# Performance work log

Hardware: AMD Instinct MI355X
Metric: run time of the kernel (lower is better)

Reference implementation:

```python
import jax, jax.numpy as jnp
import numpy as np

D_MODEL = 1024
EXPAND = 2
D_INNER = D_MODEL * EXPAND  # 2048 independent SSM channels
D_STATE = 16
BATCH = 4
SEQ = 4096


def setup_inputs() -> dict:
    key = jax.random.key(0)
    ks = jax.random.split(key, 10)
    w = lambda k, shape, scale=0.02: jax.random.normal(k, shape, jnp.float32) * scale
    return {
        "x": jax.random.normal(ks[0], (BATCH, SEQ, D_MODEL), jnp.float32),
        "w_in": w(ks[1], (D_MODEL, D_INNER)),
        "b_in": jnp.zeros((D_INNER,), jnp.float32),
        "w_gate": w(ks[2], (D_MODEL, D_INNER)),
        "b_gate": jnp.zeros((D_INNER,), jnp.float32),
        # per-channel linear SSM params: h_t = A h_{t-1} + B x_t ; y_t = C . h_t
        "A": w(ks[3], (D_INNER, D_STATE, D_STATE), 0.05),  # small spectral radius -> stable recurrence
        "B_ssm": w(ks[4], (D_INNER, D_STATE), 0.1),
        "C_ssm": w(ks[5], (D_INNER, D_STATE), 0.1),
        "w_out": w(ks[6], (D_INNER, D_MODEL)),
        "b_out": jnp.zeros((D_MODEL,), jnp.float32),
    }


def reference(x, w_in, b_in, w_gate, b_gate, A, B_ssm, C_ssm, w_out, b_out):
    # x: [B, S, D]
    x_proj = x @ w_in + b_in                     # [B, S, C]
    gate = jax.nn.sigmoid(x @ w_gate + b_gate)   # [B, S, C]

    def step(h, xt):
        # h: [B, C, N] state for all channels; xt: [B, C] scalar input per channel
        h = jnp.einsum("cnm,bcm->bcn", A, h) + B_ssm[None] * xt[:, :, None]
        y = jnp.einsum("bcn,cn->bc", h, C_ssm)
        return h, y

    h0 = jnp.zeros((x.shape[0], D_INNER, D_STATE), x.dtype)
    xs = jnp.swapaxes(x_proj, 0, 1)              # [S, B, C]
    _, ys = jax.lax.scan(step, h0, xs)           # ys: [S, B, C]
    ssm_out = jnp.swapaxes(ys, 0, 1)             # [B, S, C]

    y = ssm_out * gate
    return y @ w_out + b_out                     # [B, S, D]
```

## Files before the change

### kernel.cpp

```cpp
#include <hip/hip_runtime.h>
#include <hip/hip_bf16.h>

#define D_MODEL 1024
#define D_INNER 2048
#define D_STATE 16
#define BATCH   4
#define SEQ     4096
#define MROWS   (BATCH * SEQ)

#define LTAPS 16
#define TSPAN 64

using bf16 = __hip_bfloat16;

typedef __attribute__((ext_vector_type(8))) short bf16x8;
typedef __attribute__((ext_vector_type(4))) float f32x4;

__device__ __forceinline__ float bf2f(bf16 v) { return __bfloat162float(v); }
__device__ __forceinline__ unsigned short f2bfbits(float f) {
  bf16 h = __float2bfloat16(f);
  return *(unsigned short*)&h;
}
__device__ __forceinline__ float bfbits2f(unsigned short u) {
  union { float f; unsigned int i; } x; x.i = (unsigned int)u << 16; return x.f;
}

#define AS1CAST(p) ((const __attribute__((address_space(1))) unsigned int*)(unsigned long long)(p))
#define AS3CAST(p) ((__attribute__((address_space(3))) unsigned int*)(unsigned long long)(p))

#define FENCE() asm volatile("" ::: "memory")
#define BAR() do { FENCE(); __builtin_amdgcn_s_barrier(); FENCE(); } while (0)
#define PRIO1 __builtin_amdgcn_s_setprio(1)
#define PRIO0 __builtin_amdgcn_s_setprio(0)

#define TILE_E (256 * 64)

struct G8 {
  const bf16 *gA, *gB;
  size_t K64, K128;
  int stageLds;
  int baseA0, baseA1;
  int baseB0, baseB1;
  int wr, wc, lane;
};

__device__ __forceinline__ void g8_setup(G8& g, const bf16* A, const bf16* BT,
                                         int m0, int n0, int K)
{
  const int tid = threadIdx.x;
  g.lane = tid & 63;
  const int wv = tid >> 6;
  g.wr = wv >> 2;
  g.wc = wv & 3;
  const int lr = g.lane >> 3, sl = g.lane & 7;
  g.gA = A  + (size_t)(m0 + wv * 8 + lr) * K + (sl ^ lr) * 8;
  g.gB = BT + (size_t)(n0 + wv * 8 + lr) * K + (sl ^ lr) * 8;
  g.K64  = (size_t)64 * K;
  g.K128 = (size_t)128 * K;
  g.stageLds = wv * 8 * 64;
  const int fla = g.lane & 15, cb = g.lane >> 4;
  const int s0 = cb ^ (fla & 7), s1 = s0 ^ 4;
  g.baseA0 = (g.wr * 64 + fla) * 64 + s0 * 8;
  g.baseA1 = (g.wr * 64 + fla) * 64 + s1 * 8;
  g.baseB0 = (g.wc * 32 + fla) * 64 + s0 * 8;
  g.baseB1 = (g.wc * 32 + fla) * 64 + s1 * 8;
}

__device__ __forceinline__ void g8_stageA(const G8& g, bf16* dstTile, int h, int tau)
{
  const bf16* s = g.gA + (h ? g.K128 : (size_t)0) + (size_t)tau * 64;
  bf16* d = dstTile + g.stageLds + h * (128 * 64);
  __builtin_amdgcn_global_load_lds(AS1CAST(s), AS3CAST(d), 16, 0, 0);
  __builtin_amdgcn_global_load_lds(AS1CAST(s + g.K64), AS3CAST(d + 64 * 64), 16, 0, 0);
}

__device__ __forceinline__ void g8_stageB(const G8& g, bf16* dstTile, int h, int tau)
{
  const bf16* s = g.gB + (h ? g.K128 : (size_t)0) + (size_t)tau * 64;
  bf16* d = dstTile + g.stageLds + h * (128 * 64);
  __builtin_amdgcn_global_load_lds(AS1CAST(s), AS3CAST(d), 16, 0, 0);
  __builtin_amdgcn_global_load_lds(AS1CAST(s + g.K64), AS3CAST(d + 64 * 64), 16, 0, 0);
}

__device__ __forceinline__ void rdA(bf16x8 (&d)[4], const bf16* T, int base, int mh)
{
#pragma unroll
  for (int mi = 0; mi < 4; ++mi)
    d[mi] = *(const bf16x8*)&T[base + mh * 8192 + mi * 1024];
}
__device__ __forceinline__ void rdB(bf16x8 (&d)[2], const bf16* T, int base, int nh)
{
#pragma unroll
  for (int ni = 0; ni < 2; ++ni)
    d[ni] = *(const bf16x8*)&T[base + nh * 8192 + ni * 1024];
}

#define MQS(MH, NH, AF, BF) do { _Pragma("unroll") \
  for (int mi = 0; mi < 4; ++mi) { _Pragma("unroll") \
    for (int ni = 0; ni < 2; ++ni) \
      acc[MH][NH][mi][ni] = __builtin_amdgcn_mfma_f32_16x16x32_bf16( \
          (AF)[mi], (BF)[ni], acc[MH][NH][mi][ni], 0, 0, 0); \
  } } while (0)

template<bool MORE>
__device__ __forceinline__ void g8_tile(const G8& g, const bf16* At, const bf16* Bt,
    bf16* An, bf16* Bn, int t, f32x4 (&acc)[2][2][4][2],
    bf16x8 (&aP)[4], bf16x8 (&aQ)[4], bf16x8 (&b0s0)[2], bf16x8 (&b0s1)[2],
    bf16x8 (&b1s0)[2], bf16x8 (&b1s1)[2])
{
  rdA(aQ, At, g.baseA1, 0);
  if constexpr (MORE) g8_stageA(g, An, 0, t + 1);
  PRIO1; MQS(0, 0, aP, b0s0); PRIO0;
  rdB(b1s0, Bt, g.baseB0, 1);
  if constexpr (MORE) g8_stageB(g, Bn, 0, t + 1);
  PRIO1; MQS(0, 0, aQ, b0s1); PRIO0;
  rdB(b1s1, Bt, g.baseB1, 1);
  if constexpr (MORE) g8_stageA(g, An, 1, t + 1);
  PRIO1; MQS(0, 1, aP, b1s0); PRIO0;
  rdA(aP, At, g.baseA0, 1);
  if constexpr (MORE) g8_stageB(g, Bn, 1, t + 1);
  PRIO1; MQS(0, 1, aQ, b1s1); PRIO0;
  rdA(aQ, At, g.baseA1, 1);
  PRIO1; MQS(1, 1, aP, b1s0); PRIO0;
  PRIO1; MQS(1, 1, aQ, b1s1); PRIO0;
  PRIO1; MQS(1, 0, aP, b0s0); PRIO0;
  if constexpr (MORE) {
    asm volatile("s_waitcnt vmcnt(0)" ::: "memory");
    BAR();
  }
  PRIO1; MQS(1, 0, aQ, b0s1); PRIO0;
  if constexpr (MORE) {
    rdA(aP, An, g.baseA0, 0);
    rdB(b0s0, Bn, g.baseB0, 0);
    rdB(b0s1, Bn, g.baseB1, 0);
  }
}

__device__ __forceinline__ void g8_main(const G8& g, bf16* As, bf16* Bs,
                                        f32x4 (&acc)[2][2][4][2], int K)
{
  const int nt = K >> 6;
  bf16* A0 = As; bf16* A1 = As + TILE_E;
  bf16* B0 = Bs; bf16* B1 = Bs + TILE_E;

  g8_stageA(g, A0, 0, 0);
  g8_stageB(g, B0, 0, 0);
  g8_stageA(g, A0, 1, 0);
  g8_stageB(g, B0, 1, 0);
  asm volatile("s_waitcnt vmcnt(0)" ::: "memory");
  BAR();

  bf16x8 aP[4], aQ[4], b0s0[2], b0s1[2], b1s0[2], b1s1[2];
  rdA(aP, A0, g.baseA0, 0);
  rdB(b0s0, B0, g.baseB0, 0);
  rdB(b0s1, B0, g.baseB1, 0);

  for (int t = 0; t < nt - 1; ++t) {
    bf16* At = (t & 1) ? A1 : A0;
    bf16* Bt = (t & 1) ? B1 : B0;
    bf16* An = (t & 1) ? A0 : A1;
    bf16* Bn = (t & 1) ? B0 : B1;
    g8_tile<true>(g, At, Bt, An, Bn, t, acc, aP, aQ, b0s0, b0s1, b1s0, b1s1);
  }
  bf16* At = ((nt - 1) & 1) ? A1 : A0;
  bf16* Bt = ((nt - 1) & 1) ? B1 : B0;
  g8_tile<false>(g, At, Bt, At, Bt, nt - 1, acc, aP, aQ, b0s0, b0s1, b1s0, b1s1);
}

__global__ __launch_bounds__(512, 2) void gemm_proj_dual(
    const bf16* __restrict__ A,
    const bf16* __restrict__ BT,
    const float* __restrict__ bias_in, const float* __restrict__ bias_gate,
    bf16* __restrict__ xp, bf16* __restrict__ gate)
{
  __shared__ alignas(16) bf16 As[2 * TILE_E];
  __shared__ alignas(16) bf16 Bs[2 * TILE_E];

  const int b = blockIdx.x;
  const int swz = (b & 7) * 128 + (b >> 3);
  const int bm = swz >> 4, bn = swz & 15;
  const int m0 = bm * 256, n0 = bn * 256;

  G8 g;
  g8_setup(g, A, BT, m0, n0, D_MODEL);

  f32x4 acc[2][2][4][2];
#pragma unroll
  for (int a1 = 0; a1 < 2; ++a1)
#pragma unroll
    for (int a2 = 0; a2 < 2; ++a2)
#pragma unroll
      for (int a3 = 0; a3 < 4; ++a3)
#pragma unroll
        for (int a4 = 0; a4 < 2; ++a4)
          acc[a1][a2][a3][a4] = (f32x4){0.f, 0.f, 0.f, 0.f};

  g8_main(g, As, Bs, acc, D_MODEL);

  const bool isGate = (n0 >= D_INNER);
  const int  nloc0  = n0 - (isGate ? D_INNER : 0);
  const float* bias = isGate ? bias_gate : bias_in;
  bf16* dst         = isGate ? gate : xp;

  const int crow = (g.lane >> 4) * 4;
  const int ccol = g.lane & 15;
#pragma unroll
  for (int mh = 0; mh < 2; ++mh)
#pragma unroll
    for (int nh = 0; nh < 2; ++nh)
#pragma unroll
      for (int mi = 0; mi < 4; ++mi)
#pragma unroll
        for (int ni = 0; ni < 2; ++ni) {
          const int col = nloc0 + nh * 128 + g.wc * 32 + ni * 16 + ccol;
          const float bcol = bias[col];
#pragma unroll
          for (int r = 0; r < 4; ++r) {
            const size_t row = (size_t)(m0 + mh * 128 + g.wr * 64 + mi * 16 + crow + r);
            float v = acc[mh][nh][mi][ni][r] + bcol;
            if (isGate) v = 1.0f / (1.0f + __expf(-v));
            dst[row * D_INNER + col] = __float2bfloat16(v);
          }
        }
}

__global__ __launch_bounds__(512, 2) void gemm_out(
    const bf16* __restrict__ A,
    const bf16* __restrict__ BT,
    const float* __restrict__ bias,
    float* __restrict__ C)
{
  __shared__ alignas(16) bf16 As[2 * TILE_E];
  __shared__ alignas(16) bf16 Bs[2 * TILE_E];

  const int b = blockIdx.x;
  const int swz = (b & 7) * 32 + (b >> 3);
  const int bm = swz >> 2, bn = swz & 3;
  const int m0 = bm * 256, n0 = bn * 256;

  G8 g;
  g8_setup(g, A, BT, m0, n0, D_INNER);

  f32x4 acc[2][2][4][2];
#pragma unroll
  for (int a1 = 0; a1 < 2; ++a1)
#pragma unroll
    for (int a2 = 0; a2 < 2; ++a2)
#pragma unroll
      for (int a3 = 0; a3 < 4; ++a3)
#pragma unroll
        for (int a4 = 0; a4 < 2; ++a4)
          acc[a1][a2][a3][a4] = (f32x4){0.f, 0.f, 0.f, 0.f};

  g8_main(g, As, Bs, acc, D_INNER);

  const int crow = (g.lane >> 4) * 4;
  const int ccol = g.lane & 15;
#pragma unroll
  for (int mh = 0; mh < 2; ++mh)
#pragma unroll
    for (int nh = 0; nh < 2; ++nh)
#pragma unroll
      for (int mi = 0; mi < 4; ++mi)
#pragma unroll
        for (int ni = 0; ni < 2; ++ni) {
          const int col = n0 + nh * 128 + g.wc * 32 + ni * 16 + ccol;
          const float bcol = bias[col];
#pragma unroll
          for (int r = 0; r < 4; ++r) {
            const size_t row = (size_t)(m0 + mh * 128 + g.wr * 64 + mi * 16 + crow + r);
            C[row * D_MODEL + col] = acc[mh][nh][mi][ni][r] + bcol;
          }
        }
}

__global__ __launch_bounds__(256) void f32_to_bf16(
    const float* __restrict__ in, bf16* __restrict__ out, int n4)
{
  const int i = (blockIdx.x * 256 + threadIdx.x);
  if (i >= n4) return;
  const float4 v = *(const float4*)(in + (size_t)i * 4);
  ushort4 r;
  r.x = f2bfbits(v.x); r.y = f2bfbits(v.y); r.z = f2bfbits(v.z); r.w = f2bfbits(v.w);
  *(ushort4*)(out + (size_t)i * 4) = r;
}

__global__ __launch_bounds__(256) void transpose_to_bf16(
    const float* __restrict__ in, bf16* __restrict__ out, int R, int C)
{
  __shared__ float tile[32][33];
  const int c0 = blockIdx.x * 32, r0 = blockIdx.y * 32;
  const int tx = threadIdx.x & 31, ty = threadIdx.x >> 5;
#pragma unroll
  for (int i = ty; i < 32; i += 8)
    tile[i][tx] = in[(size_t)(r0 + i) * C + c0 + tx];
  __syncthreads();
#pragma unroll
  for (int i = ty; i < 32; i += 8)
    out[(size_t)(c0 + i) * R + r0 + tx] = __float2bfloat16(tile[tx][i]);
}

__device__ __forceinline__ float4 load4f(const float* p) { return *(const float4*)p; }

__global__ __launch_bounds__(256) void ssm_taps(
    const float* __restrict__ A, const float* __restrict__ Bv,
    const float* __restrict__ Cv, float* __restrict__ g)
{
  const int c = blockIdx.x * blockDim.x + threadIdx.x;
  if (c >= D_INNER) return;
  const float* Ac = A + (size_t)c * D_STATE * D_STATE;
  float v[D_STATE], cr[D_STATE];
#pragma unroll
  for (int i = 0; i < D_STATE; ++i) {
    v[i]  = Bv[(size_t)c * D_STATE + i];
    cr[i] = Cv[(size_t)c * D_STATE + i];
  }
  for (int m = 0; m < LTAPS; ++m) {
    float y = 0.f;
#pragma unroll
    for (int i = 0; i < D_STATE; ++i) y += cr[i] * v[i];
    g[(size_t)m * D_INNER + c] = y;
    float nv[D_STATE];
#pragma unroll
    for (int n = 0; n < D_STATE; ++n) {
      const float4 a0 = load4f(Ac + n * D_STATE + 0);
      const float4 a1 = load4f(Ac + n * D_STATE + 4);
      const float4 a2 = load4f(Ac + n * D_STATE + 8);
      const float4 a3 = load4f(Ac + n * D_STATE + 12);
      float s = a0.x * v[0] + a0.y * v[1] + a0.z * v[2] + a0.w * v[3];
      s += a1.x * v[4] + a1.y * v[5] + a1.z * v[6] + a1.w * v[7];
      s += a2.x * v[8] + a2.y * v[9] + a2.z * v[10] + a2.w * v[11];
      s += a3.x * v[12] + a3.y * v[13] + a3.z * v[14] + a3.w * v[15];
      nv[n] = s;
    }
#pragma unroll
    for (int i = 0; i < D_STATE; ++i) v[i] = nv[i];
  }
}

__global__ __launch_bounds__(256) void conv_gate(
    const bf16* __restrict__ xp, bf16* __restrict__ gate_io,
    const float* __restrict__ g)
{
  const int cp = blockIdx.x * blockDim.x + threadIdx.x;
  const int c  = cp * 2;
  const int b  = blockIdx.z;
  const int t0 = blockIdx.y * TSPAN;

  float gg0[LTAPS], gg1[LTAPS];
#pragma unroll
  for (int m = 0; m < LTAPS; ++m) {
    gg0[m] = g[(size_t)m * D_INNER + c];
    gg1[m] = g[(size_t)m * D_INNER + c + 1];
  }

  const size_t baseBC = ((size_t)b * SEQ) * D_INNER + c;

  float w0[2 * LTAPS], w1[2 * LTAPS];
#pragma unroll
  for (int j = 0; j < LTAPS; ++j) {
    const int t = t0 - LTAPS + j;
    if (t >= 0) {
      const ushort2 v = *(const ushort2*)&xp[baseBC + (size_t)t * D_INNER];
      w0[j] = bfbits2f(v.x); w1[j] = bfbits2f(v.y);
    } else { w0[j] = 0.f; w1[j] = 0.f; }
  }

  for (int blk = 0; blk < TSPAN; blk += LTAPS) {
#pragma unroll
    for (int j = 0; j < LTAPS; ++j) {
      const ushort2 v = *(const ushort2*)&xp[baseBC + (size_t)(t0 + blk + j) * D_INNER];
      w0[LTAPS + j] = bfbits2f(v.x); w1[LTAPS + j] = bfbits2f(v.y);
    }
#pragma unroll
    for (int j = 0; j < LTAPS; ++j) {
      float y0 = 0.f, y1 = 0.f;
#pragma unroll
      for (int m = 0; m < LTAPS; ++m) {
        y0 += gg0[m] * w0[LTAPS + j - m];
        y1 += gg1[m] * w1[LTAPS + j - m];
      }
      const size_t idx = baseBC + (size_t)(t0 + blk + j) * D_INNER;
      const unsigned int gv = *(const unsigned int*)&gate_io[idx];
      const float g0 = bfbits2f((unsigned short)(gv & 0xffffu));
      const float g1 = bfbits2f((unsigned short)(gv >> 16));
      const unsigned int ov =
          (unsigned int)f2bfbits(y0 * g0) | ((unsigned int)f2bfbits(y1 * g1) << 16);
      *(unsigned int*)&gate_io[idx] = ov;
    }
#pragma unroll
    for (int j = 0; j < LTAPS; ++j) { w0[j] = w0[j + LTAPS]; w1[j] = w1[j + LTAPS]; }
  }
}

extern "C" void kernel_launch(void* const* d_in, const int* in_sizes, int n_in,
                              void* d_out, int out_size, void* d_ws, size_t ws_size,
                              hipStream_t stream)
{
  const float* x      = (const float*)d_in[0];
  const float* w_in   = (const float*)d_in[1];
  const float* b_in   = (const float*)d_in[2];
  const float* w_gate = (const float*)d_in[3];
  const float* b_gate = (const float*)d_in[4];
  const float* A      = (const float*)d_in[5];
  const float* B_ssm  = (const float*)d_in[6];
  const float* C_ssm  = (const float*)d_in[7];
  const float* w_out  = (const float*)d_in[8];
  const float* b_out  = (const float*)d_in[9];
  float* out = (float*)d_out;

  char* ws = (char*)d_ws;
  bf16*  gate  = (bf16*)(ws);
  bf16*  xbf   = (bf16*)(ws + 67108864);
  bf16*  wcatT = (bf16*)(ws + 100663296);
  bf16*  w_otT = (bf16*)(ws + 109051904);
  float* taps  = (float*)(ws + 113246208);
  bf16*  xp    = (bf16*)d_out;

  dim3 blk(256);

  hipLaunchKernelGGL(ssm_taps, dim3(D_INNER / 256), blk, 0, stream, A, B_ssm, C_ssm, taps);
  hipLaunchKernelGGL(f32_to_bf16, dim3((MROWS * D_MODEL / 4) / 256), blk, 0, stream,
                     x, xbf, MROWS * D_MODEL / 4);
  hipLaunchKernelGGL(transpose_to_bf16, dim3(D_INNER / 32, D_MODEL / 32), blk, 0, stream,
                     w_in, wcatT, D_MODEL, D_INNER);
  hipLaunchKernelGGL(transpose_to_bf16, dim3(D_INNER / 32, D_MODEL / 32), blk, 0, stream,
                     w_gate, wcatT + (size_t)D_INNER * D_MODEL, D_MODEL, D_INNER);
  hipLaunchKernelGGL(transpose_to_bf16, dim3(D_MODEL / 32, D_INNER / 32), blk, 0, stream,
                     w_out, w_otT, D_INNER, D_MODEL);

  dim3 gblk(512);
  hipLaunchKernelGGL(gemm_proj_dual, dim3((2 * D_INNER / 256) * (MROWS / 256)), gblk, 0, stream,
                     xbf, wcatT, b_in, b_gate, xp, gate);

  dim3 gc(D_INNER / 2 / 256, SEQ / TSPAN, BATCH);
  hipLaunchKernelGGL(conv_gate, gc, blk, 0, stream, xp, gate, taps);

  hipLaunchKernelGGL(gemm_out, dim3((D_MODEL / 256) * (MROWS / 256)), gblk, 0, stream,
                     gate, w_otT, b_out, out);
}
```

Before: 391.0 us.

## Load GEMM B fragments directly from global into registers with 4-stage A ring

Both GEMM kernels stop staging the B operand through LDS and instead load each wave's B fragments straight from global memory into registers one K-step ahead. The A tile gets a 4-deep LDS ring with a prefetch distance of two, and a barrier only every second K-step. Launch bounds drop to one block per CU. The aim is to halve LDS traffic and cut barriers, at the cost of uncoalesced, redundant global reads of B across waves, higher register pressure and lower occupancy.

```diff
diff --git a/kernel.cpp b/kernel.cpp
--- a/kernel.cpp
+++ b/kernel.cpp
@@ -33,14 +33,14 @@
 #define PRIO1 __builtin_amdgcn_s_setprio(1)
 #define PRIO0 __builtin_amdgcn_s_setprio(0)
 
-#define TILE_E (256 * 64)
+#define TILE_A 16384
 
 struct G8 {
-  const bf16 *gA, *gB;
-  size_t K64, K128;
+  const bf16 *gA;
+  const bf16 *gBF;
+  size_t K64;
   int stageLds;
   int baseA0, baseA1;
-  int baseB0, baseB1;
   int wr, wc, lane;
 };
 
@@ -53,33 +53,35 @@
   g.wr = wv >> 2;
   g.wc = wv & 3;
   const int lr = g.lane >> 3, sl = g.lane & 7;
-  g.gA = A  + (size_t)(m0 + wv * 8 + lr) * K + (sl ^ lr) * 8;
-  g.gB = BT + (size_t)(n0 + wv * 8 + lr) * K + (sl ^ lr) * 8;
-  g.K64  = (size_t)64 * K;
-  g.K128 = (size_t)128 * K;
+  g.gA = A + (size_t)(m0 + wv * 8 + lr) * K + (sl ^ lr) * 8;
+  g.K64 = (size_t)64 * K;
   g.stageLds = wv * 8 * 64;
   const int fla = g.lane & 15, cb = g.lane >> 4;
-  const int s0 = cb ^ (fla & 7), s1 = s0 ^ 4;
+  const int s0 = cb ^ (fla & 7);
   g.baseA0 = (g.wr * 64 + fla) * 64 + s0 * 8;
-  g.baseA1 = (g.wr * 64 + fla) * 64 + s1 * 8;
-  g.baseB0 = (g.wc * 32 + fla) * 64 + s0 * 8;
-  g.baseB1 = (g.wc * 32 + fla) * 64 + s1 * 8;
-}
-
-__device__ __forceinline__ void g8_stageA(const G8& g, bf16* dstTile, int h, int tau)
-{
-  const bf16* s = g.gA + (h ? g.K128 : (size_t)0) + (size_t)tau * 64;
-  bf16* d = dstTile + g.stageLds + h * (128 * 64);
-  __builtin_amdgcn_global_load_lds(AS1CAST(s), AS3CAST(d), 16, 0, 0);
-  __builtin_amdgcn_global_load_lds(AS1CAST(s + g.K64), AS3CAST(d + 64 * 64), 16, 0, 0);
-}
-
-__device__ __forceinline__ void g8_stageB(const G8& g, bf16* dstTile, int h, int tau)
-{
-  const bf16* s = g.gB + (h ? g.K128 : (size_t)0) + (size_t)tau * 64;
-  bf16* d = dstTile + g.stageLds + h * (128 * 64);
-  __builtin_amdgcn_global_load_lds(AS1CAST(s), AS3CAST(d), 16, 0, 0);
-  __builtin_amdgcn_global_load_lds(AS1CAST(s + g.K64), AS3CAST(d + 64 * 64), 16, 0, 0);
+  g.baseA1 = (g.wr * 64 + fla) * 64 + (s0 ^ 4) * 8;
+  g.gBF = BT + (size_t)(n0 + g.wc * 32 + fla) * K + cb * 8;
+}
+
+__device__ __forceinline__ void g8_stageA(const G8& g, bf16* dstTile, int tau)
+{
+  const bf16* s = g.gA + (size_t)tau * 64;
+  bf16* d = dstTile + g.stageLds;
+  __builtin_amdgcn_global_load_lds(AS1CAST(s),             AS3CAST(d),         16, 0, 0);
+  __builtin_amdgcn_global_load_lds(AS1CAST(s + g.K64),     AS3CAST(d + 4096),  16, 0, 0);
+  __builtin_amdgcn_global_load_lds(AS1CAST(s + 2 * g.K64), AS3CAST(d + 8192),  16, 0, 0);
+  __builtin_amdgcn_global_load_lds(AS1CAST(s + 3 * g.K64), AS3CAST(d + 12288), 16, 0, 0);
+}
+
+template<int S>
+__device__ __forceinline__ void loadBs(const G8& g, bf16x8 (&B)[2][2][2], int t, int K)
+{
+#pragma unroll
+  for (int nh = 0; nh < 2; ++nh)
+#pragma unroll
+    for (int ni = 0; ni < 2; ++ni)
+      B[S][nh][ni] = *(const bf16x8*)(g.gBF + (size_t)(nh * 128 + ni * 16) * K
+                                      + (size_t)t * 64 + S * 32);
 }
 
 __device__ __forceinline__ void rdA(bf16x8 (&d)[4], const bf16* T, int base, int mh)
@@ -88,93 +90,71 @@
   for (int mi = 0; mi < 4; ++mi)
     d[mi] = *(const bf16x8*)&T[base + mh * 8192 + mi * 1024];
 }
-__device__ __forceinline__ void rdB(bf16x8 (&d)[2], const bf16* T, int base, int nh)
-{
-#pragma unroll
-  for (int ni = 0; ni < 2; ++ni)
-    d[ni] = *(const bf16x8*)&T[base + nh * 8192 + ni * 1024];
-}
-
-#define MQS(MH, NH, AF, BF) do { _Pragma("unroll") \
-  for (int mi = 0; mi < 4; ++mi) { _Pragma("unroll") \
-    for (int ni = 0; ni < 2; ++ni) \
-      acc[MH][NH][mi][ni] = __builtin_amdgcn_mfma_f32_16x16x32_bf16( \
-          (AF)[mi], (BF)[ni], acc[MH][NH][mi][ni], 0, 0, 0); \
-  } } while (0)
-
-template<bool MORE>
-__device__ __forceinline__ void g8_tile(const G8& g, const bf16* At, const bf16* Bt,
-    bf16* An, bf16* Bn, int t, f32x4 (&acc)[2][2][4][2],
-    bf16x8 (&aP)[4], bf16x8 (&aQ)[4], bf16x8 (&b0s0)[2], bf16x8 (&b0s1)[2],
-    bf16x8 (&b1s0)[2], bf16x8 (&b1s1)[2])
-{
-  rdA(aQ, At, g.baseA1, 0);
-  if constexpr (MORE) g8_stageA(g, An, 0, t + 1);
-  PRIO1; MQS(0, 0, aP, b0s0); PRIO0;
-  rdB(b1s0, Bt, g.baseB0, 1);
-  if constexpr (MORE) g8_stageB(g, Bn, 0, t + 1);
-  PRIO1; MQS(0, 0, aQ, b0s1); PRIO0;
-  rdB(b1s1, Bt, g.baseB1, 1);
-  if constexpr (MORE) g8_stageA(g, An, 1, t + 1);
-  PRIO1; MQS(0, 1, aP, b1s0); PRIO0;
-  rdA(aP, At, g.baseA0, 1);
-  if constexpr (MORE) g8_stageB(g, Bn, 1, t + 1);
-  PRIO1; MQS(0, 1, aQ, b1s1); PRIO0;
-  rdA(aQ, At, g.baseA1, 1);
-  PRIO1; MQS(1, 1, aP, b1s0); PRIO0;
-  PRIO1; MQS(1, 1, aQ, b1s1); PRIO0;
-  PRIO1; MQS(1, 0, aP, b0s0); PRIO0;
-  if constexpr (MORE) {
-    asm volatile("s_waitcnt vmcnt(0)" ::: "memory");
-    BAR();
-  }
-  PRIO1; MQS(1, 0, aQ, b0s1); PRIO0;
-  if constexpr (MORE) {
-    rdA(aP, An, g.baseA0, 0);
-    rdB(b0s0, Bn, g.baseB0, 0);
-    rdB(b0s1, Bn, g.baseB1, 0);
-  }
-}
-
-__device__ __forceinline__ void g8_main(const G8& g, bf16* As, bf16* Bs,
+
+#define MQ2(MH, S, AF, BB) do { _Pragma("unroll") \
+  for (int nh = 0; nh < 2; ++nh) { _Pragma("unroll") \
+    for (int mi = 0; mi < 4; ++mi) { _Pragma("unroll") \
+      for (int ni = 0; ni < 2; ++ni) \
+        acc[MH][nh][mi][ni] = __builtin_amdgcn_mfma_f32_16x16x32_bf16( \
+            (AF)[mi], (BB)[S][nh][ni], acc[MH][nh][mi][ni], 0, 0, 0); \
+  } } } while (0)
+
+template<bool LB, bool ST, bool BARR, bool NXT, int BCUR, int BSTG, int BNXT>
+__device__ __forceinline__ void g8_t(const G8& g, bf16* As, int t, int K,
+    f32x4 (&acc)[2][2][4][2], bf16x8 (&aP)[4], bf16x8 (&aQ)[4],
+    bf16x8 (&Bb)[2][2][2])
+{
+  const bf16* Tc = As + BCUR;
+  rdA(aQ, Tc, g.baseA1, 0);
+  if constexpr (ST) g8_stageA(g, As + BSTG, t + 2);
+  PRIO1; MQ2(0, 0, aP, Bb); PRIO0;
+  rdA(aP, Tc, g.baseA0, 1);
+  PRIO1; MQ2(0, 1, aQ, Bb); PRIO0;
+  rdA(aQ, Tc, g.baseA1, 1);
+  PRIO1; MQ2(1, 0, aP, Bb); PRIO0;
+  if constexpr (LB) loadBs<0>(g, Bb, t + 1, K);
+  if constexpr (BARR) { asm volatile("s_waitcnt vmcnt(0)" ::: "memory"); BAR(); }
+  PRIO1; MQ2(1, 1, aQ, Bb); PRIO0;
+  if constexpr (LB) loadBs<1>(g, Bb, t + 1, K);
+  if constexpr (NXT) rdA(aP, As + BNXT, g.baseA0, 0);
+}
+
+__device__ __forceinline__ void g8_main(const G8& g, bf16* As,
                                         f32x4 (&acc)[2][2][4][2], int K)
 {
   const int nt = K >> 6;
-  bf16* A0 = As; bf16* A1 = As + TILE_E;
-  bf16* B0 = Bs; bf16* B1 = Bs + TILE_E;
-
-  g8_stageA(g, A0, 0, 0);
-  g8_stageB(g, B0, 0, 0);
-  g8_stageA(g, A0, 1, 0);
-  g8_stageB(g, B0, 1, 0);
+  bf16x8 Bb[2][2][2];
+
+  g8_stageA(g, As,          0);
+  g8_stageA(g, As + TILE_A, 1);
+  loadBs<0>(g, Bb, 0, K);
+  loadBs<1>(g, Bb, 0, K);
   asm volatile("s_waitcnt vmcnt(0)" ::: "memory");
   BAR();
 
-  bf16x8 aP[4], aQ[4], b0s0[2], b0s1[2], b1s0[2], b1s1[2];
-  rdA(aP, A0, g.baseA0, 0);
-  rdB(b0s0, B0, g.baseB0, 0);
-  rdB(b0s1, B0, g.baseB1, 0);
-
-  for (int t = 0; t < nt - 1; ++t) {
-    bf16* At = (t & 1) ? A1 : A0;
-    bf16* Bt = (t & 1) ? B1 : B0;
-    bf16* An = (t & 1) ? A0 : A1;
-    bf16* Bn = (t & 1) ? B0 : B1;
-    g8_tile<true>(g, At, Bt, An, Bn, t, acc, aP, aQ, b0s0, b0s1, b1s0, b1s1);
-  }
-  bf16* At = ((nt - 1) & 1) ? A1 : A0;
-  bf16* Bt = ((nt - 1) & 1) ? B1 : B0;
-  g8_tile<false>(g, At, Bt, At, Bt, nt - 1, acc, aP, aQ, b0s0, b0s1, b1s0, b1s1);
-}
-
-__global__ __launch_bounds__(512, 2) void gemm_proj_dual(
+  bf16x8 aP[4], aQ[4];
+  rdA(aP, As, g.baseA0, 0);
+
+  int t = 0;
+  for (; t < nt - 4; t += 4) {
+    g8_t<true, true, false, true, 0,     32768, 16384>(g, As, t + 0, K, acc, aP, aQ, Bb);
+    g8_t<true, true, true,  true, 16384, 49152, 32768>(g, As, t + 1, K, acc, aP, aQ, Bb);
+    g8_t<true, true, false, true, 32768, 0,     49152>(g, As, t + 2, K, acc, aP, aQ, Bb);
+    g8_t<true, true, true,  true, 49152, 16384, 0    >(g, As, t + 3, K, acc, aP, aQ, Bb);
+  }
+  g8_t<true,  true,  false, true,  0,     32768, 16384>(g, As, t + 0, K, acc, aP, aQ, Bb);
+  g8_t<true,  true,  true,  true,  16384, 49152, 32768>(g, As, t + 1, K, acc, aP, aQ, Bb);
+  g8_t<true,  false, false, true,  32768, 0,     49152>(g, As, t + 2, K, acc, aP, aQ, Bb);
+  g8_t<false, false, false, false, 49152, 0,     0    >(g, As, t + 3, K, acc, aP, aQ, Bb);
+}
+
+__global__ __launch_bounds__(512, 1) void gemm_proj_dual(
     const bf16* __restrict__ A,
     const bf16* __restrict__ BT,
     const float* __restrict__ bias_in, const float* __restrict__ bias_gate,
     bf16* __restrict__ xp, bf16* __restrict__ gate)
 {
-  __shared__ alignas(16) bf16 As[2 * TILE_E];
-  __shared__ alignas(16) bf16 Bs[2 * TILE_E];
+  __shared__ alignas(16) bf16 As[4 * TILE_A];
 
   const int b = blockIdx.x;
   const int swz = (b & 7) * 128 + (b >> 3);
@@ -195,7 +175,7 @@
         for (int a4 = 0; a4 < 2; ++a4)
           acc[a1][a2][a3][a4] = (f32x4){0.f, 0.f, 0.f, 0.f};
 
-  g8_main(g, As, Bs, acc, D_MODEL);
+  g8_main(g, As, acc, D_MODEL);
 
   const bool isGate = (n0 >= D_INNER);
   const int  nloc0  = n0 - (isGate ? D_INNER : 0);
@@ -224,14 +204,13 @@
         }
 }
 
-__global__ __launch_bounds__(512, 2) void gemm_out(
+__global__ __launch_bounds__(512, 1) void gemm_out(
     const bf16* __restrict__ A,
     const bf16* __restrict__ BT,
     const float* __restrict__ bias,
     float* __restrict__ C)
 {
-  __shared__ alignas(16) bf16 As[2 * TILE_E];
-  __shared__ alignas(16) bf16 Bs[2 * TILE_E];
+  __shared__ alignas(16) bf16 As[4 * TILE_A];
 
   const int b = blockIdx.x;
   const int swz = (b & 7) * 32 + (b >> 3);
@@ -252,7 +231,7 @@
         for (int a4 = 0; a4 < 2; ++a4)
           acc[a1][a2][a3][a4] = (f32x4){0.f, 0.f, 0.f, 0.f};
 
-  g8_main(g, As, Bs, acc, D_INNER);
+  g8_main(g, As, acc, D_INNER);
 
   const int crow = (g.lane >> 4) * 4;
   const int ccol = g.lane & 15;
```

After: 478.3 us. 1.22x slower.

## Fuse weight transposes and SSM taps into one prep kernel; reorder GEMM prefetch

Applied to the files above, without the earlier changes.

Merges the three weight transpose launches and the SSM tap computation into a single kernel that picks its role from the block index, cutting launch overhead and the idle tail between small kernels. Separately, inside the GEMM main loop, both halves of the next A and B tiles are now issued at the start of each tile instead of being interleaved across the MFMA groups. This puts global loads in flight earlier, at the cost of more outstanding loads competing with LDS reads at the start of each tile.

```diff
diff --git a/kernel.cpp b/kernel.cpp
--- a/kernel.cpp
+++ b/kernel.cpp
@@ -109,16 +109,14 @@
     bf16x8 (&b1s0)[2], bf16x8 (&b1s1)[2])
 {
   rdA(aQ, At, g.baseA1, 0);
-  if constexpr (MORE) g8_stageA(g, An, 0, t + 1);
+  if constexpr (MORE) { g8_stageA(g, An, 0, t + 1); g8_stageA(g, An, 1, t + 1); }
   PRIO1; MQS(0, 0, aP, b0s0); PRIO0;
   rdB(b1s0, Bt, g.baseB0, 1);
-  if constexpr (MORE) g8_stageB(g, Bn, 0, t + 1);
+  if constexpr (MORE) { g8_stageB(g, Bn, 0, t + 1); g8_stageB(g, Bn, 1, t + 1); }
   PRIO1; MQS(0, 0, aQ, b0s1); PRIO0;
   rdB(b1s1, Bt, g.baseB1, 1);
-  if constexpr (MORE) g8_stageA(g, An, 1, t + 1);
   PRIO1; MQS(0, 1, aP, b1s0); PRIO0;
   rdA(aP, At, g.baseA0, 1);
-  if constexpr (MORE) g8_stageB(g, Bn, 1, t + 1);
   PRIO1; MQS(0, 1, aQ, b1s1); PRIO0;
   rdA(aQ, At, g.baseA1, 1);
   PRIO1; MQS(1, 1, aP, b1s0); PRIO0;
@@ -144,8 +142,8 @@
   bf16* B0 = Bs; bf16* B1 = Bs + TILE_E;
 
   g8_stageA(g, A0, 0, 0);
+  g8_stageA(g, A0, 1, 0);
   g8_stageB(g, B0, 0, 0);
-  g8_stageA(g, A0, 1, 0);
   g8_stageB(g, B0, 1, 0);
   asm volatile("s_waitcnt vmcnt(0)" ::: "memory");
   BAR();
@@ -285,11 +283,14 @@
   *(ushort4*)(out + (size_t)i * 4) = r;
 }
 
-__global__ __launch_bounds__(256) void transpose_to_bf16(
-    const float* __restrict__ in, bf16* __restrict__ out, int R, int C)
-{
-  __shared__ float tile[32][33];
-  const int c0 = blockIdx.x * 32, r0 = blockIdx.y * 32;
+__device__ __forceinline__ float4 load4f(const float* p) { return *(const float4*)p; }
+
+__device__ __forceinline__ void transpose_body(
+    const float* __restrict__ in, bf16* __restrict__ out, int R, int C,
+    int idx, float (*tile)[33])
+{
+  const int nbx = C / 32;
+  const int c0 = (idx % nbx) * 32, r0 = (idx / nbx) * 32;
   const int tx = threadIdx.x & 31, ty = threadIdx.x >> 5;
 #pragma unroll
   for (int i = ty; i < 32; i += 8)
@@ -300,41 +301,54 @@
     out[(size_t)(c0 + i) * R + r0 + tx] = __float2bfloat16(tile[tx][i]);
 }
 
-__device__ __forceinline__ float4 load4f(const float* p) { return *(const float4*)p; }
-
-__global__ __launch_bounds__(256) void ssm_taps(
+__global__ __launch_bounds__(256) void prep_wt(
+    const float* __restrict__ w_in, const float* __restrict__ w_gate,
+    const float* __restrict__ w_out,
     const float* __restrict__ A, const float* __restrict__ Bv,
-    const float* __restrict__ Cv, float* __restrict__ g)
-{
-  const int c = blockIdx.x * blockDim.x + threadIdx.x;
-  if (c >= D_INNER) return;
-  const float* Ac = A + (size_t)c * D_STATE * D_STATE;
-  float v[D_STATE], cr[D_STATE];
-#pragma unroll
-  for (int i = 0; i < D_STATE; ++i) {
-    v[i]  = Bv[(size_t)c * D_STATE + i];
-    cr[i] = Cv[(size_t)c * D_STATE + i];
-  }
-  for (int m = 0; m < LTAPS; ++m) {
-    float y = 0.f;
-#pragma unroll
-    for (int i = 0; i < D_STATE; ++i) y += cr[i] * v[i];
-    g[(size_t)m * D_INNER + c] = y;
-    float nv[D_STATE];
-#pragma unroll
-    for (int n = 0; n < D_STATE; ++n) {
-      const float4 a0 = load4f(Ac + n * D_STATE + 0);
-      const float4 a1 = load4f(Ac + n * D_STATE + 4);
-      const float4 a2 = load4f(Ac + n * D_STATE + 8);
-      const float4 a3 = load4f(Ac + n * D_STATE + 12);
-      float s = a0.x * v[0] + a0.y * v[1] + a0.z * v[2] + a0.w * v[3];
-      s += a1.x * v[4] + a1.y * v[5] + a1.z * v[6] + a1.w * v[7];
-      s += a2.x * v[8] + a2.y * v[9] + a2.z * v[10] + a2.w * v[11];
-      s += a3.x * v[12] + a3.y * v[13] + a3.z * v[14] + a3.w * v[15];
-      nv[n] = s;
+    const float* __restrict__ Cv,
+    bf16* __restrict__ wcatT, bf16* __restrict__ w_otT,
+    float* __restrict__ taps)
+{
+  __shared__ float tile[32][33];
+  const int bid = blockIdx.x;
+  if (bid < 2048) {
+    transpose_body(w_in, wcatT, D_MODEL, D_INNER, bid, tile);
+  } else if (bid < 4096) {
+    transpose_body(w_gate, wcatT + (size_t)D_INNER * D_MODEL, D_MODEL, D_INNER,
+                   bid - 2048, tile);
+  } else if (bid < 6144) {
+    transpose_body(w_out, w_otT, D_INNER, D_MODEL, bid - 4096, tile);
+  } else {
+    const int c = (bid - 6144) * 256 + threadIdx.x;
+    if (c >= D_INNER) return;
+    const float* Ac = A + (size_t)c * D_STATE * D_STATE;
+    float v[D_STATE], cr[D_STATE];
+#pragma unroll
+    for (int i = 0; i < D_STATE; ++i) {
+      v[i]  = Bv[(size_t)c * D_STATE + i];
+      cr[i] = Cv[(size_t)c * D_STATE + i];
     }
-#pragma unroll
-    for (int i = 0; i < D_STATE; ++i) v[i] = nv[i];
+    for (int m = 0; m < LTAPS; ++m) {
+      float y = 0.f;
+#pragma unroll
+      for (int i = 0; i < D_STATE; ++i) y += cr[i] * v[i];
+      taps[(size_t)m * D_INNER + c] = y;
+      float nv[D_STATE];
+#pragma unroll
+      for (int n = 0; n < D_STATE; ++n) {
+        const float4 a0 = load4f(Ac + n * D_STATE + 0);
+        const float4 a1 = load4f(Ac + n * D_STATE + 4);
+        const float4 a2 = load4f(Ac + n * D_STATE + 8);
+        const float4 a3 = load4f(Ac + n * D_STATE + 12);
+        float s = a0.x * v[0] + a0.y * v[1] + a0.z * v[2] + a0.w * v[3];
+        s += a1.x * v[4] + a1.y * v[5] + a1.z * v[6] + a1.w * v[7];
+        s += a2.x * v[8] + a2.y * v[9] + a2.z * v[10] + a2.w * v[11];
+        s += a3.x * v[12] + a3.y * v[13] + a3.z * v[14] + a3.w * v[15];
+        nv[n] = s;
+      }
+#pragma unroll
+      for (int i = 0; i < D_STATE; ++i) v[i] = nv[i];
+    }
   }
 }
 
@@ -417,24 +431,17 @@
   float* taps  = (float*)(ws + 113246208);
   bf16*  xp    = (bf16*)d_out;
 
-  dim3 blk(256);
-
-  hipLaunchKernelGGL(ssm_taps, dim3(D_INNER / 256), blk, 0, stream, A, B_ssm, C_ssm, taps);
-  hipLaunchKernelGGL(f32_to_bf16, dim3((MROWS * D_MODEL / 4) / 256), blk, 0, stream,
+  hipLaunchKernelGGL(f32_to_bf16, dim3((MROWS * D_MODEL / 4) / 256), dim3(256), 0, stream,
                      x, xbf, MROWS * D_MODEL / 4);
-  hipLaunchKernelGGL(transpose_to_bf16, dim3(D_INNER / 32, D_MODEL / 32), blk, 0, stream,
-                     w_in, wcatT, D_MODEL, D_INNER);
-  hipLaunchKernelGGL(transpose_to_bf16, dim3(D_INNER / 32, D_MODEL / 32), blk, 0, stream,
-                     w_gate, wcatT + (size_t)D_INNER * D_MODEL, D_MODEL, D_INNER);
-  hipLaunchKernelGGL(transpose_to_bf16, dim3(D_MODEL / 32, D_INNER / 32), blk, 0, stream,
-                     w_out, w_otT, D_INNER, D_MODEL);
+  hipLaunchKernelGGL(prep_wt, dim3(6152), dim3(256), 0, stream,
+                     w_in, w_gate, w_out, A, B_ssm, C_ssm, wcatT, w_otT, taps);
 
   dim3 gblk(512);
   hipLaunchKernelGGL(gemm_proj_dual, dim3((2 * D_INNER / 256) * (MROWS / 256)), gblk, 0, stream,
                      xbf, wcatT, b_in, b_gate, xp, gate);
 
   dim3 gc(D_INNER / 2 / 256, SEQ / TSPAN, BATCH);
-  hipLaunchKernelGGL(conv_gate, gc, blk, 0, stream, xp, gate, taps);
+  hipLaunchKernelGGL(conv_gate, gc, dim3(256), 0, stream, xp, gate, taps);
 
   hipLaunchKernelGGL(gemm_out, dim3((D_MODEL / 256) * (MROWS / 256)), gblk, 0, stream,
                      gate, w_otT, b_out, out);
```

Measured after the change: 443.9 us. +13.5%, slower.
